# Kernel optimization log

Measured on AMD Instinct MI355X. Metric: run time of the kernel, lower is better.

Reference implementation:

```python
import jax, jax.numpy as jnp
import numpy as np

N = 50000   # num_nodes
E = 1600000 # edges (avg degree 32)
D = 256     # in_feats
H = 256     # n_hidden


def setup_inputs() -> dict:
    key = jax.random.key(0)
    ks = jax.random.split(key, 9)
    s = 1.0 / np.sqrt(D)
    return {
        "input_nodes": jnp.arange(N, dtype=jnp.int32),
        "edge_src": jax.random.randint(ks[0], (E,), 0, N, dtype=jnp.int32),
        "edge_dst": jax.random.randint(ks[1], (E,), 0, N, dtype=jnp.int32),
        "emb": jax.random.normal(ks[2], (N, D), jnp.float32) * 0.02,
        "W_self0": jax.random.normal(ks[3], (D, H), jnp.float32) * s,
        "W_neigh0": jax.random.normal(ks[4], (D, H), jnp.float32) * s,
        "b0": jnp.zeros((H,), jnp.float32),
        "W_self1": jax.random.normal(ks[5], (H, H), jnp.float32) * s,
        "W_neigh1": jax.random.normal(ks[6], (H, H), jnp.float32) * s,
        "b1": jnp.zeros((H,), jnp.float32),
    }


def _sage_mean(h, src, dst, W_self, W_neigh, b, n):
    # gather neighbor features, mean-reduce by destination, then linear.
    msgs = h[src]                                                  # [E, d]
    ssum = jax.ops.segment_sum(msgs, dst, num_segments=n)          # [n, d]
    deg = jax.ops.segment_sum(jnp.ones(src.shape, h.dtype), dst, num_segments=n)
    h_neigh = ssum / jnp.maximum(deg, 1.0)[:, None]
    return h @ W_self + h_neigh @ W_neigh + b


def reference(input_nodes, edge_src, edge_dst, emb,
              W_self0, W_neigh0, b0, W_self1, W_neigh1, b1):
    h = emb[input_nodes]                                            # [N, D]
    h = _sage_mean(h, edge_src, edge_dst, W_self0, W_neigh0, b0, N)
    h = jax.nn.relu(h)  # dropout is identity at inference
    h = _sage_mean(h, edge_src, edge_dst, W_self1, W_neigh1, b1, N)
    h = h / jnp.linalg.norm(h)  # global Frobenius norm, as in torch.norm(h)
    return h
```

## Files before the change

kernel.cpp:

```cpp
#include <hip/hip_runtime.h>
#include <math.h>

#define NN 50000
#define NE 1600000
#define DF 256
#define NBUCK 391
#define CHS ((long long)NN * 32)

typedef unsigned short ushortT;
typedef __attribute__((ext_vector_type(8))) short short8;
typedef __attribute__((ext_vector_type(4))) float floatx4;
typedef __attribute__((ext_vector_type(4))) unsigned uintx4;

__device__ __forceinline__ unsigned bf16rne(float f) {
    unsigned u = __float_as_uint(f);
    return (u + 0x7fffu + ((u >> 16) & 1u)) >> 16;
}

#define ASYNC16(gptr, ldsptr) \
    __builtin_amdgcn_global_load_lds((const __attribute__((address_space(1))) unsigned*)(gptr), \
                                     (__attribute__((address_space(3))) unsigned*)(ldsptr), 16, 0, 0)


__global__ void k_zero(int* __restrict__ bcnt) {
    int i = blockIdx.x * 256 + threadIdx.x;
    if (i < NBUCK) bcnt[i] = 0;
}

__global__ __launch_bounds__(256)
void k_bhist(const int* __restrict__ dst, int* __restrict__ bcnt) {
    __shared__ int h[NBUCK];
    for (int i = threadIdx.x; i < NBUCK; i += 256) h[i] = 0;
    __syncthreads();
    int base = blockIdx.x * 4096;
#pragma unroll
    for (int i = 0; i < 16; ++i) {
        int e = base + i * 256 + threadIdx.x;
        if (e < NE) atomicAdd(&h[dst[e] >> 7], 1);
    }
    __syncthreads();
    for (int i = threadIdx.x; i < NBUCK; i += 256)
        if (h[i]) atomicAdd(&bcnt[i], h[i]);
}

__global__ void k_bscan(const int* __restrict__ bcnt, int* __restrict__ bbase,
                        int* __restrict__ cursor, int* __restrict__ row_ptr,
                        float* __restrict__ nrm) {
    __shared__ int s[512];
    int t = threadIdx.x;
    int v = (t < NBUCK) ? bcnt[t] : 0;
    s[t] = v; __syncthreads();
    for (int off = 1; off < 512; off <<= 1) {
        int x = (t >= off) ? s[t - off] : 0;
        __syncthreads();
        s[t] += x;
        __syncthreads();
    }
    if (t < NBUCK) { bbase[t] = s[t] - v; cursor[t] = s[t] - v; }
    if (t == 0) { bbase[NBUCK] = NE; row_ptr[NN] = NE; *nrm = 0.0f; }
}

__global__ __launch_bounds__(256)
void k_bin(const int* __restrict__ src, const int* __restrict__ dst,
           int* __restrict__ cursor, unsigned* __restrict__ rec) {
    __shared__ int h[NBUCK];
    __shared__ int gb[NBUCK];
    for (int i = threadIdx.x; i < NBUCK; i += 256) h[i] = 0;
    __syncthreads();
    const int base = blockIdx.x * 2048;
    int bk[8], rk[8];
    unsigned pk[8];
#pragma unroll
    for (int i = 0; i < 8; ++i) {
        int e = base + i * 256 + threadIdx.x;
        if (e < NE) {
            int d = dst[e];
            bk[i] = d >> 7;
            pk[i] = (unsigned)src[e] | ((unsigned)(d & 127) << 16);
            rk[i] = atomicAdd(&h[bk[i]], 1);
        } else bk[i] = -1;
    }
    __syncthreads();
    for (int i = threadIdx.x; i < NBUCK; i += 256) {
        int c = h[i];
        gb[i] = c ? atomicAdd(&cursor[i], c) : 0;
    }
    __syncthreads();
#pragma unroll
    for (int i = 0; i < 8; ++i)
        if (bk[i] >= 0) rec[gb[bk[i]] + rk[i]] = pk[i];
}

__global__ __launch_bounds__(256)
void k_csr(const unsigned* __restrict__ rec, const int* __restrict__ bbase,
           int* __restrict__ row_ptr, ushortT* __restrict__ csr) {
    __shared__ int cnt[128];
    __shared__ int cur[128];
    __shared__ int s[256];
    const int B = blockIdx.x, t = threadIdx.x;
    if (t < 128) cnt[t] = 0;
    __syncthreads();
    const int beg = bbase[B], end = bbase[B + 1];
    for (int p = beg + t; p < end; p += 256)
        atomicAdd(&cnt[(rec[p] >> 16) & 127], 1);
    __syncthreads();
    int v = (t < 128) ? cnt[t] : 0;
    s[t] = v; __syncthreads();
    for (int off = 1; off < 256; off <<= 1) {
        int x = (t >= off) ? s[t - off] : 0;
        __syncthreads();
        s[t] += x;
        __syncthreads();
    }
    if (t < 128) {
        int ex = s[t] - v;
        cur[t] = ex;
        int node = B * 128 + t;
        if (node < NN) row_ptr[node] = beg + ex;
    }
    __syncthreads();
    for (int p = beg + t; p < end; p += 256) {
        unsigned r = rec[p];
        int loc = atomicAdd(&cur[(r >> 16) & 127], 1);
        csr[beg + loc] = (ushortT)r;
    }
}


__global__ __launch_bounds__(256)
void k_cvt(const float* __restrict__ emb, const int* __restrict__ gather,
           ushortT* __restrict__ embb,
           const float* __restrict__ Ws0, const float* __restrict__ Wn0,
           ushortT* __restrict__ Wt0,
           const float* __restrict__ Ws1, const float* __restrict__ Wn1,
           ushortT* __restrict__ Wt1) {
    const int b = blockIdx.x;
    if (b < 6250) {
        long long i = ((long long)b * 256 + threadIdx.x) * 8;
        int row = (int)(i >> 8);
        int col = (int)(i & 255);
        long long g = (long long)gather[row] * 256 + col;
        float4 v0 = *(const float4*)(emb + g);
        float4 v1 = *(const float4*)(emb + g + 4);
        uint4 o;
        o.x = bf16rne(v0.x) | (bf16rne(v0.y) << 16);
        o.y = bf16rne(v0.z) | (bf16rne(v0.w) << 16);
        o.z = bf16rne(v1.x) | (bf16rne(v1.y) << 16);
        o.w = bf16rne(v1.z) | (bf16rne(v1.w) << 16);
        *(uint4*)(embb + ((long long)(col >> 5) * NN + row) * 32 + (col & 31)) = o;
    } else {
        const bool first = b < 6762;
        const int idx = ((first ? b - 6250 : b - 6762)) * 256 + threadIdx.x;
        const int n = idx >> 9;
        const int k = idx & 511;
        const float* Ws = first ? Ws0 : Ws1;
        const float* Wn = first ? Wn0 : Wn1;
        float v = (k < 256) ? Ws[k * 256 + n] : Wn[(k - 256) * 256 + n];
        (first ? Wt0 : Wt1)[idx] = (ushortT)bf16rne(v);
    }
}


__global__ __launch_bounds__(256)
void k_agg(const ushortT* __restrict__ feat, const int* __restrict__ row_ptr,
           const ushortT* __restrict__ csr, ushortT* __restrict__ out) {
    const int c    = blockIdx.x & 7;
    const int ng   = blockIdx.x >> 3;
    const int node = ng * 64 + (threadIdx.x >> 2);
    const int part = (threadIdx.x & 3) * 8;
    if (node >= NN) return;

    const ushortT* fc = feat + (long long)c * CHS;
    const int beg = row_ptr[node], end = row_ptr[node + 1];

    float s[8] = {0.f, 0.f, 0.f, 0.f, 0.f, 0.f, 0.f, 0.f};

#define ACCUM(q) do { \
        s[0] += __uint_as_float(q.x << 16); \
        s[1] += __uint_as_float(q.x & 0xffff0000u); \
        s[2] += __uint_as_float(q.y << 16); \
        s[3] += __uint_as_float(q.y & 0xffff0000u); \
        s[4] += __uint_as_float(q.z << 16); \
        s[5] += __uint_as_float(q.z & 0xffff0000u); \
        s[6] += __uint_as_float(q.w << 16); \
        s[7] += __uint_as_float(q.w & 0xffff0000u); \
    } while (0)

    int p = beg;

    if (p < end && (p & 1)) {
        int i0 = (int)__builtin_nontemporal_load(csr + p);
        uintx4 q = *(const uintx4*)(fc + i0 * 32 + part);
        ACCUM(q);
        ++p;
    }

    unsigned x0 = 0, x1 = 0, x2 = 0, x3 = 0;
    if (p + 7 < end) {
        const unsigned* cp = (const unsigned*)(csr + p);
        x0 = __builtin_nontemporal_load(cp + 0);
        x1 = __builtin_nontemporal_load(cp + 1);
        x2 = __builtin_nontemporal_load(cp + 2);
        x3 = __builtin_nontemporal_load(cp + 3);
    }

    while (p + 7 < end) {
        uintx4 q0 = *(const uintx4*)(fc + (int)(x0 & 0xffffu) * 32 + part);
        uintx4 q1 = *(const uintx4*)(fc + (int)(x0 >> 16)     * 32 + part);
        uintx4 q2 = *(const uintx4*)(fc + (int)(x1 & 0xffffu) * 32 + part);
        uintx4 q3 = *(const uintx4*)(fc + (int)(x1 >> 16)     * 32 + part);
        uintx4 q4 = *(const uintx4*)(fc + (int)(x2 & 0xffffu) * 32 + part);
        uintx4 q5 = *(const uintx4*)(fc + (int)(x2 >> 16)     * 32 + part);
        uintx4 q6 = *(const uintx4*)(fc + (int)(x3 & 0xffffu) * 32 + part);
        uintx4 q7 = *(const uintx4*)(fc + (int)(x3 >> 16)     * 32 + part);

        const int np = p + 8;
        if (np + 7 < end) {
            const unsigned* cp = (const unsigned*)(csr + np);
            x0 = __builtin_nontemporal_load(cp + 0);
            x1 = __builtin_nontemporal_load(cp + 1);
            x2 = __builtin_nontemporal_load(cp + 2);
            x3 = __builtin_nontemporal_load(cp + 3);
        }

        ACCUM(q0); ACCUM(q1); ACCUM(q2); ACCUM(q3);
        ACCUM(q4); ACCUM(q5); ACCUM(q6); ACCUM(q7);
        p = np;
    }

    for (; p < end; ++p) {
        int i0 = (int)__builtin_nontemporal_load(csr + p);
        uintx4 q = *(const uintx4*)(fc + i0 * 32 + part);
        ACCUM(q);
    }
#undef ACCUM

    float inv = 1.0f / fmaxf((float)(end - beg), 1.0f);
    uintx4 o;
    o.x = bf16rne(s[0] * inv) | (bf16rne(s[1] * inv) << 16);
    o.y = bf16rne(s[2] * inv) | (bf16rne(s[3] * inv) << 16);
    o.z = bf16rne(s[4] * inv) | (bf16rne(s[5] * inv) << 16);
    o.w = bf16rne(s[6] * inv) | (bf16rne(s[7] * inv) << 16);
    __builtin_nontemporal_store(o, (uintx4*)(out + ((long long)c * NN + node) * 32 + part));
}


template<int RELU, int NORM>
__global__ __launch_bounds__(256, 4)
void k_gemm(const ushortT* __restrict__ Aself, const ushortT* __restrict__ Aneigh,
            const ushortT* __restrict__ Wt, const float* __restrict__ bias,
            ushortT* __restrict__ Cb, float* __restrict__ Cf, float* __restrict__ norm_acc) {
    __shared__ ushortT As[2048];
    __shared__ ushortT Bs[8192];
    __shared__ float red[4];

    const int t = threadIdx.x;
    const int w = t >> 6;
    const int lane = t & 63;
    const int m0 = blockIdx.x * 64;

    const int ar = t >> 2;
    const int cu = (t & 3) * 8;

    const long long gA = (long long)min(m0 + ar, NN - 1) * 32 + cu;

    const unsigned ldsA = w * 512;
    const unsigned ldsB = w * 512;

    const int fm = lane & 15;
    const int fk = (lane >> 4) * 8;

    floatx4 acc[4][4];
#pragma unroll
    for (int i = 0; i < 4; ++i)
#pragma unroll
        for (int j = 0; j < 4; ++j) acc[i][j] = (floatx4){0.f, 0.f, 0.f, 0.f};

    for (int kt = 0; kt < 512; kt += 32) {
        const ushortT* Ab = (kt < 256)
            ? (Aself  + (long long)(kt >> 5) * CHS)
            : (Aneigh + (long long)((kt - 256) >> 5) * CHS);

        __syncthreads();
        ASYNC16(Ab + gA, As + ldsA);
#pragma unroll
        for (int i = 0; i < 4; ++i)
            ASYNC16(Wt + (i * 64 + ar) * 512 + kt + cu, Bs + i * 2048 + ldsB);
        __syncthreads();

        short8 af[4], bf[4];
#pragma unroll
        for (int i = 0; i < 4; ++i)
            af[i] = *(const short8*)&As[(i * 16 + fm) * 32 + fk];
#pragma unroll
        for (int j = 0; j < 4; ++j)
            bf[j] = *(const short8*)&Bs[(w * 64 + j * 16 + fm) * 32 + fk];
#pragma unroll
        for (int i = 0; i < 4; ++i)
#pragma unroll
            for (int j = 0; j < 4; ++j)
                acc[i][j] = __builtin_amdgcn_mfma_f32_16x16x32_bf16(af[i], bf[j], acc[i][j], 0, 0, 0);
    }

    float bj[4];
#pragma unroll
    for (int j = 0; j < 4; ++j) bj[j] = bias[w * 64 + j * 16 + fm];

    float sumsq = 0.0f;
#pragma unroll
    for (int i = 0; i < 4; ++i) {
#pragma unroll
        for (int r = 0; r < 4; ++r) {
            const int row = m0 + i * 16 + (lane >> 4) * 4 + r;
            if (row < NN) {
#pragma unroll
                for (int j = 0; j < 4; ++j) {
                    const int col = w * 64 + j * 16 + fm;
                    float v = acc[i][j][r] + bj[j];
                    if (RELU) v = fmaxf(v, 0.0f);
                    if (NORM) {
                        Cf[(long long)row * 256 + col] = v;
                        sumsq += v * v;
                    } else {
                        Cb[((long long)(col >> 5) * NN + row) * 32 + (col & 31)] = (ushortT)bf16rne(v);
                    }
                }
            }
        }
    }

    if (NORM) {
#pragma unroll
        for (int off = 32; off > 0; off >>= 1) sumsq += __shfl_down(sumsq, off);
        if (lane == 0) red[w] = sumsq;
        __syncthreads();
        if (t == 0) atomicAdd(norm_acc, red[0] + red[1] + red[2] + red[3]);
    }
}

__global__ void k_scale(float* __restrict__ out, const float* __restrict__ nrm) {
    const float s = 1.0f / sqrtf(*nrm);
    long long i = ((long long)blockIdx.x * 256 + threadIdx.x) * 4;
    float4 v = *(float4*)&out[i];
    v.x *= s; v.y *= s; v.z *= s; v.w *= s;
    *(float4*)&out[i] = v;
}


extern "C" void kernel_launch(void* const* d_in, const int* in_sizes, int n_in,
                              void* d_out, int out_size, void* d_ws, size_t ws_size,
                              hipStream_t stream) {
    const int*   input_nodes = (const int*)d_in[0];
    const int*   esrc = (const int*)d_in[1];
    const int*   edst = (const int*)d_in[2];
    const float* emb  = (const float*)d_in[3];
    const float* Ws0  = (const float*)d_in[4];
    const float* Wn0  = (const float*)d_in[5];
    const float* b0   = (const float*)d_in[6];
    const float* Ws1  = (const float*)d_in[7];
    const float* Wn1  = (const float*)d_in[8];
    const float* b1   = (const float*)d_in[9];
    float* out = (float*)d_out;

    char* base = (char*)d_ws;
    ushortT*  embb    = (ushortT*) (base);
    ushortT*  h1b     = (ushortT*) (base + 25600000);
    ushortT*  hnb     = (ushortT*) (base + 51200000);
    unsigned* rec     = (unsigned*)(base + 76800000);
    ushortT*  csr     = (ushortT*) (base + 83200000);
    ushortT*  Wt0     = (ushortT*) (base + 86400000);
    ushortT*  Wt1     = (ushortT*) (base + 86662144);
    int*      row_ptr = (int*)     (base + 86924288);
    int*      bcnt    = (int*)     (base + 87124304);
    int*      bbase   = (int*)     (base + 87125904);
    int*      cursor  = (int*)     (base + 87127504);
    float*    nrm     = (float*)   (base + 87129104);

    k_zero  <<<2,     256, 0, stream>>>(bcnt);
    k_bhist <<<391,   256, 0, stream>>>(edst, bcnt);
    k_bscan <<<1,     512, 0, stream>>>(bcnt, bbase, cursor, row_ptr, nrm);
    k_bin   <<<782,   256, 0, stream>>>(esrc, edst, cursor, rec);
    k_csr   <<<NBUCK, 256, 0, stream>>>(rec, bbase, row_ptr, csr);

    k_cvt<<<7274, 256, 0, stream>>>(emb, input_nodes, embb, Ws0, Wn0, Wt0, Ws1, Wn1, Wt1);

    const int GEMM_BLOCKS = (NN + 63) / 64;
    const int AGG_BLOCKS  = GEMM_BLOCKS * 8;

    k_agg<<<AGG_BLOCKS, 256, 0, stream>>>(embb, row_ptr, csr, hnb);
    k_gemm<1, 0><<<GEMM_BLOCKS, 256, 0, stream>>>(embb, hnb, Wt0, b0, h1b, nullptr, nullptr);

    k_agg<<<AGG_BLOCKS, 256, 0, stream>>>(h1b, row_ptr, csr, hnb);
    k_gemm<0, 1><<<GEMM_BLOCKS, 256, 0, stream>>>(h1b, hnb, Wt1, b1, nullptr, out, nrm);

    k_scale<<<NN * DF / 4 / 256, 256, 0, stream>>>(out, nrm);
}
```

Measured before the change: 517.2 us.

## Widen feature chunks to 64 columns and sort CSR neighbors by source half

```diff
diff --git a/kernel.cpp b/kernel.cpp
--- a/kernel.cpp
+++ b/kernel.cpp
@@ -5,7 +5,8 @@
 #define NE 1600000
 #define DF 256
 #define NBUCK 391
-#define CHS ((long long)NN * 32)
+#define CHS4 ((long long)NN * 64)
+#define HALFN 25000
 
 typedef unsigned short ushortT;
 typedef __attribute__((ext_vector_type(8))) short short8;
@@ -91,20 +92,24 @@
         if (bk[i] >= 0) rec[gb[bk[i]] + rk[i]] = pk[i];
 }
 
+
 __global__ __launch_bounds__(256)
 void k_csr(const unsigned* __restrict__ rec, const int* __restrict__ bbase,
            int* __restrict__ row_ptr, ushortT* __restrict__ csr) {
-    __shared__ int cnt[128];
-    __shared__ int cur[128];
+    __shared__ int cnt[256];
+    __shared__ int cur[256];
     __shared__ int s[256];
     const int B = blockIdx.x, t = threadIdx.x;
-    if (t < 128) cnt[t] = 0;
+    cnt[t] = 0;
     __syncthreads();
     const int beg = bbase[B], end = bbase[B + 1];
-    for (int p = beg + t; p < end; p += 256)
-        atomicAdd(&cnt[(rec[p] >> 16) & 127], 1);
-    __syncthreads();
-    int v = (t < 128) ? cnt[t] : 0;
+    for (int p = beg + t; p < end; p += 256) {
+        unsigned r = rec[p];
+        int idx = (int)((r >> 16) & 127) * 2 + ((r & 0xffffu) >= HALFN ? 1 : 0);
+        atomicAdd(&cnt[idx], 1);
+    }
+    __syncthreads();
+    int v = cnt[t];
     s[t] = v; __syncthreads();
     for (int off = 1; off < 256; off <<= 1) {
         int x = (t >= off) ? s[t - off] : 0;
@@ -112,16 +117,16 @@
         s[t] += x;
         __syncthreads();
     }
+    cur[t] = s[t] - v;
+    __syncthreads();
     if (t < 128) {
-        int ex = s[t] - v;
-        cur[t] = ex;
         int node = B * 128 + t;
-        if (node < NN) row_ptr[node] = beg + ex;
-    }
-    __syncthreads();
+        if (node < NN) row_ptr[node] = beg + cur[2 * t];
+    }
     for (int p = beg + t; p < end; p += 256) {
         unsigned r = rec[p];
-        int loc = atomicAdd(&cur[(r >> 16) & 127], 1);
+        int idx = (int)((r >> 16) & 127) * 2 + ((r & 0xffffu) >= HALFN ? 1 : 0);
+        int loc = atomicAdd(&cur[idx], 1);
         csr[beg + loc] = (ushortT)r;
     }
 }
@@ -147,7 +152,7 @@
         o.y = bf16rne(v0.z) | (bf16rne(v0.w) << 16);
         o.z = bf16rne(v1.x) | (bf16rne(v1.y) << 16);
         o.w = bf16rne(v1.z) | (bf16rne(v1.w) << 16);
-        *(uint4*)(embb + ((long long)(col >> 5) * NN + row) * 32 + (col & 31)) = o;
+        *(uint4*)(embb + ((long long)(col >> 6) * NN + row) * 64 + (col & 63)) = o;
     } else {
         const bool first = b < 6762;
         const int idx = ((first ? b - 6250 : b - 6762)) * 256 + threadIdx.x;
@@ -164,13 +169,13 @@
 __global__ __launch_bounds__(256)
 void k_agg(const ushortT* __restrict__ feat, const int* __restrict__ row_ptr,
            const ushortT* __restrict__ csr, ushortT* __restrict__ out) {
-    const int c    = blockIdx.x & 7;
-    const int ng   = blockIdx.x >> 3;
-    const int node = ng * 64 + (threadIdx.x >> 2);
-    const int part = (threadIdx.x & 3) * 8;
+    const int c    = blockIdx.x & 3;
+    const int ng   = blockIdx.x >> 2;
+    const int node = ng * 32 + (threadIdx.x >> 3);
+    const int part = (threadIdx.x & 7) * 8;
     if (node >= NN) return;
 
-    const ushortT* fc = feat + (long long)c * CHS;
+    const ushortT* fc = feat + (long long)c * CHS4;
     const int beg = row_ptr[node], end = row_ptr[node + 1];
 
     float s[8] = {0.f, 0.f, 0.f, 0.f, 0.f, 0.f, 0.f, 0.f};
@@ -190,7 +195,7 @@
 
     if (p < end && (p & 1)) {
         int i0 = (int)__builtin_nontemporal_load(csr + p);
-        uintx4 q = *(const uintx4*)(fc + i0 * 32 + part);
+        uintx4 q = *(const uintx4*)(fc + i0 * 64 + part);
         ACCUM(q);
         ++p;
     }
@@ -205,14 +210,14 @@
     }
 
     while (p + 7 < end) {
-        uintx4 q0 = *(const uintx4*)(fc + (int)(x0 & 0xffffu) * 32 + part);
-        uintx4 q1 = *(const uintx4*)(fc + (int)(x0 >> 16)     * 32 + part);
-        uintx4 q2 = *(const uintx4*)(fc + (int)(x1 & 0xffffu) * 32 + part);
-        uintx4 q3 = *(const uintx4*)(fc + (int)(x1 >> 16)     * 32 + part);
-        uintx4 q4 = *(const uintx4*)(fc + (int)(x2 & 0xffffu) * 32 + part);
-        uintx4 q5 = *(const uintx4*)(fc + (int)(x2 >> 16)     * 32 + part);
-        uintx4 q6 = *(const uintx4*)(fc + (int)(x3 & 0xffffu) * 32 + part);
-        uintx4 q7 = *(const uintx4*)(fc + (int)(x3 >> 16)     * 32 + part);
+        uintx4 q0 = *(const uintx4*)(fc + (int)(x0 & 0xffffu) * 64 + part);
+        uintx4 q1 = *(const uintx4*)(fc + (int)(x0 >> 16)     * 64 + part);
+        uintx4 q2 = *(const uintx4*)(fc + (int)(x1 & 0xffffu) * 64 + part);
+        uintx4 q3 = *(const uintx4*)(fc + (int)(x1 >> 16)     * 64 + part);
+        uintx4 q4 = *(const uintx4*)(fc + (int)(x2 & 0xffffu) * 64 + part);
+        uintx4 q5 = *(const uintx4*)(fc + (int)(x2 >> 16)     * 64 + part);
+        uintx4 q6 = *(const uintx4*)(fc + (int)(x3 & 0xffffu) * 64 + part);
+        uintx4 q7 = *(const uintx4*)(fc + (int)(x3 >> 16)     * 64 + part);
 
         const int np = p + 8;
         if (np + 7 < end) {
@@ -230,7 +235,7 @@
 
     for (; p < end; ++p) {
         int i0 = (int)__builtin_nontemporal_load(csr + p);
-        uintx4 q = *(const uintx4*)(fc + i0 * 32 + part);
+        uintx4 q = *(const uintx4*)(fc + i0 * 64 + part);
         ACCUM(q);
     }
 #undef ACCUM
@@ -241,7 +246,7 @@
     o.y = bf16rne(s[2] * inv) | (bf16rne(s[3] * inv) << 16);
     o.z = bf16rne(s[4] * inv) | (bf16rne(s[5] * inv) << 16);
     o.w = bf16rne(s[6] * inv) | (bf16rne(s[7] * inv) << 16);
-    __builtin_nontemporal_store(o, (uintx4*)(out + ((long long)c * NN + node) * 32 + part));
+    __builtin_nontemporal_store(o, (uintx4*)(out + ((long long)c * NN + node) * 64 + part));
 }
 
 
@@ -262,7 +267,7 @@
     const int ar = t >> 2;
     const int cu = (t & 3) * 8;
 
-    const long long gA = (long long)min(m0 + ar, NN - 1) * 32 + cu;
+    const long long gA = (long long)min(m0 + ar, NN - 1) * 64 + cu;
 
     const unsigned ldsA = w * 512;
     const unsigned ldsB = w * 512;
@@ -277,9 +282,9 @@
         for (int j = 0; j < 4; ++j) acc[i][j] = (floatx4){0.f, 0.f, 0.f, 0.f};
 
     for (int kt = 0; kt < 512; kt += 32) {
-        const ushortT* Ab = (kt < 256)
-            ? (Aself  + (long long)(kt >> 5) * CHS)
-            : (Aneigh + (long long)((kt - 256) >> 5) * CHS);
+        const int kc = (kt < 256) ? kt : kt - 256;
+        const ushortT* Ab = ((kt < 256) ? Aself : Aneigh)
+                          + (long long)(kc >> 6) * CHS4 + (kc & 32);
 
         __syncthreads();
         ASYNC16(Ab + gA, As + ldsA);
@@ -322,7 +327,7 @@
                         Cf[(long long)row * 256 + col] = v;
                         sumsq += v * v;
                     } else {
-                        Cb[((long long)(col >> 5) * NN + row) * 32 + (col & 31)] = (ushortT)bf16rne(v);
+                        Cb[((long long)(col >> 6) * NN + row) * 64 + (col & 63)] = (ushortT)bf16rne(v);
                     }
                 }
             }
@@ -385,7 +390,7 @@
     k_cvt<<<7274, 256, 0, stream>>>(emb, input_nodes, embb, Ws0, Wn0, Wt0, Ws1, Wn1, Wt1);
 
     const int GEMM_BLOCKS = (NN + 63) / 64;
-    const int AGG_BLOCKS  = GEMM_BLOCKS * 8;
+    const int AGG_BLOCKS  = ((NN + 31) / 32) * 4;
 
     k_agg<<<AGG_BLOCKS, 256, 0, stream>>>(embb, row_ptr, csr, hnb);
     k_gemm<1, 0><<<GEMM_BLOCKS, 256, 0, stream>>>(embb, hnb, Wt0, b0, h1b, nullptr, nullptr);
```

After: 453.8 us. 1.14x faster.
